# Kernel optimization log

Measured on AMD Instinct MI355X. Metric: run time of the kernel, lower is better.

## Reference

```python
import jax, jax.numpy as jnp
import numpy as np

B, T, H = 32, 512, 1024
I = 1024  # input_size == hidden_size


def _init_lstm(key, in_dim, hid):
    # PyTorch nn.LSTM init: U(-k, k), k = 1/sqrt(hidden_size)
    k = 1.0 / np.sqrt(hid)
    ks = jax.random.split(key, 4)
    Wih = jax.random.uniform(ks[0], (4 * hid, in_dim), minval=-k, maxval=k, dtype=jnp.float32)
    Whh = jax.random.uniform(ks[1], (4 * hid, hid), minval=-k, maxval=k, dtype=jnp.float32)
    bih = jax.random.uniform(ks[2], (4 * hid,), minval=-k, maxval=k, dtype=jnp.float32)
    bhh = jax.random.uniform(ks[3], (4 * hid,), minval=-k, maxval=k, dtype=jnp.float32)
    return Wih, Whh, bih, bhh


def setup_inputs() -> dict:
    key = jax.random.key(0)
    kx, k0, k1 = jax.random.split(key, 3)
    x = jax.random.normal(kx, (B, T, I), dtype=jnp.float32)
    Wih0, Whh0, bih0, bhh0 = _init_lstm(k0, I, H)
    Wih1, Whh1, bih1, bhh1 = _init_lstm(k1, H, H)
    return {"x": x, "Wih0": Wih0, "Whh0": Whh0, "bih0": bih0, "bhh0": bhh0,
            "Wih1": Wih1, "Whh1": Whh1, "bih1": bih1, "bhh1": bhh1}


def _lstm_layer(x, Wih, Whh, bih, bhh):
    # x: [B, T, in_dim] -> h_seq: [B, T, H]. PyTorch gate order: i, f, g, o.
    hid = Whh.shape[1]
    # Precompute input projections for all timesteps (one big GEMM).
    xg = jnp.einsum('bti,gi->btg', x, Wih) + bih + bhh  # [B, T, 4H]
    xg = jnp.swapaxes(xg, 0, 1)  # [T, B, 4H] for scan over time

    def step(carry, xg_t):
        h, c = carry
        gates = xg_t + h @ Whh.T  # [B, 4H]
        i, f, g, o = jnp.split(gates, 4, axis=-1)
        i = jax.nn.sigmoid(i)
        f = jax.nn.sigmoid(f)
        g = jnp.tanh(g)
        o = jax.nn.sigmoid(o)
        c = f * c + i * g
        h = o * jnp.tanh(c)
        return (h, c), h

    h0 = jnp.zeros((x.shape[0], hid), dtype=x.dtype)
    c0 = jnp.zeros((x.shape[0], hid), dtype=x.dtype)
    _, h_seq = jax.lax.scan(step, (h0, c0), xg)
    return jnp.swapaxes(h_seq, 0, 1)  # [B, T, H]


def reference(x, Wih0, Whh0, bih0, bhh0, Wih1, Whh1, bih1, bhh1):
    # Layer 0
    h = _lstm_layer(x, Wih0, Whh0, bih0, bhh0)
    # Layer 1 with residual add (dropout p=0.0 -> identity)
    h = h + _lstm_layer(h, Wih1, Whh1, bih1, bhh1)
    return h
```

## Files before the change

### kernel.cpp

```cpp
#include <hip/hip_runtime.h>
#include <hip/hip_bf16.h>

#define BB 32
#define TT 512
#define HH 1024
#define II 1024
#define G4H 4096
#define BH  (BB * HH)
#define HD  8
#define HMASK (HD - 1)

typedef __bf16 bf16x8_t __attribute__((ext_vector_type(8)));
typedef float f32x4_t __attribute__((ext_vector_type(4)));
typedef int i32x4_t __attribute__((ext_vector_type(4)));
typedef unsigned long long u64;

__device__ __forceinline__ void gload16(const void* g, void* l) {
    __builtin_amdgcn_global_load_lds(
        (const __attribute__((address_space(1))) unsigned int*)g,
        (__attribute__((address_space(3))) unsigned int*)l, 16, 0, 0);
}

__global__ void init_bufs(unsigned* __restrict__ h0w, unsigned* __restrict__ h1w,
                          unsigned* __restrict__ cnt) {
    int i = blockIdx.x * 256 + threadIdx.x;
    if (i < 16384)
        __hip_atomic_store(h0w + i, 0u, __ATOMIC_RELAXED, __HIP_MEMORY_SCOPE_AGENT);
    else if (i < 32768)
        __hip_atomic_store(h1w + (i - 16384), 0u, __ATOMIC_RELAXED, __HIP_MEMORY_SCOPE_AGENT);
    else if (i < 49152)
        __hip_atomic_store(cnt + (i - 32768), 0u, __ATOMIC_RELAXED, __HIP_MEMORY_SCOPE_AGENT);
}

__global__ void shuffle_w(const float* __restrict__ src, __hip_bfloat16* __restrict__ dst) {
    size_t i = (size_t)blockIdx.x * 256 + threadIdx.x;
    int jj   = (int)(i & 7);
    int lane = (int)((i >> 3) & 63);
    int kb   = (int)((i >> 9) & 15);
    int kh   = (int)((i >> 13) & 1);
    int tau  = (int)((i >> 14) & 1);
    int hg   = (int)(i >> 15);
    int n = lane & 15, q = lane >> 4;
    int row = (2 * tau + (n >> 3)) * 1024 + hg * 8 + (n & 7);
    int col = kh * 512 + kb * 32 + q * 8 + jj;
    dst[i] = __float2bfloat16(src[(size_t)row * II + col]);
}

__global__ void convert_x(const float* __restrict__ x, __hip_bfloat16* __restrict__ xb) {
    size_t i = (size_t)blockIdx.x * 256 + threadIdx.x;
    int ii = (int)(i & 1023);
    int b  = (int)((i >> 10) & 31);
    int t  = (int)(i >> 15);
    xb[i] = __float2bfloat16(x[((size_t)b * TT + t) * II + ii]);
}

__global__ __launch_bounds__(512, 2)
void lstm_persist(const __hip_bfloat16* __restrict__ xb,
                  const __hip_bfloat16* __restrict__ Wxs0, const __hip_bfloat16* __restrict__ Whs0,
                  const __hip_bfloat16* __restrict__ Wxs1, const __hip_bfloat16* __restrict__ Whs1,
                  const float* __restrict__ bih0, const float* __restrict__ bhh0,
                  const float* __restrict__ bih1, const float* __restrict__ bhh1,
                  __hip_bfloat16* __restrict__ h0seq,
                  __hip_bfloat16* __restrict__ h1seq,
                  float* __restrict__ out,
                  unsigned* __restrict__ cnt)
{
    const int wg = blockIdx.x, tid = threadIdx.x;
    const int bh = wg >> 7, hg = wg & 127;
    const int wave = tid >> 6, lane = tid & 63;
    const int L = wave >> 2, p = (wave >> 1) & 1, kh = wave & 1;
    const int n = lane & 15, q = lane >> 4;

    __shared__ float psum[2][2][2][16][37];
    __shared__ float res[2][128];
    __shared__ __align__(16) unsigned short hstage[2][16][8];
    __shared__ float houtf[16][8];
    __shared__ __align__(16) char astage[6 * 16384];

    const __hip_bfloat16* Wsel = L ? (p ? Whs1 : Wxs1) : (p ? Whs0 : Wxs0);
    const __bf16* wbp = (const __bf16*)Wsel;

    i32x4_t W0, W1, W2, W3, W4, W5, W6, W7, W8, W9, W10, W11, W12, W13, W14, W15,
            W16, W17, W18, W19, W20, W21, W22, W23, W24, W25, W26, W27, W28, W29, W30, W31;
#define LOADW(IDX, TAU, KB) \
    W##IDX = *(const i32x4_t*)(const void*)(wbp + ((((((size_t)hg * 2 + (TAU)) * 2 + kh) * 16) + (KB)) * 64 + lane) * 8)
    LOADW(0,0,0);  LOADW(1,0,1);  LOADW(2,0,2);  LOADW(3,0,3);
    LOADW(4,0,4);  LOADW(5,0,5);  LOADW(6,0,6);  LOADW(7,0,7);
    LOADW(8,0,8);  LOADW(9,0,9);  LOADW(10,0,10); LOADW(11,0,11);
    LOADW(12,0,12); LOADW(13,0,13); LOADW(14,0,14); LOADW(15,0,15);
    LOADW(16,1,0);  LOADW(17,1,1);  LOADW(18,1,2);  LOADW(19,1,3);
    LOADW(20,1,4);  LOADW(21,1,5);  LOADW(22,1,6);  LOADW(23,1,7);
    LOADW(24,1,8);  LOADW(25,1,9);  LOADW(26,1,10); LOADW(27,1,11);
    LOADW(28,1,12); LOADW(29,1,13); LOADW(30,1,14); LOADW(31,1,15);
#undef LOADW
    asm volatile("" : "+v"(W0), "+v"(W1), "+v"(W2), "+v"(W3),
                      "+v"(W4), "+v"(W5), "+v"(W6), "+v"(W7));
    asm volatile("" : "+v"(W8), "+v"(W9), "+v"(W10), "+v"(W11),
                      "+v"(W12), "+v"(W13), "+v"(W14), "+v"(W15));
    asm volatile("" : "+v"(W16), "+v"(W17), "+v"(W18), "+v"(W19),
                      "+v"(W20), "+v"(W21), "+v"(W22), "+v"(W23));
    asm volatile("" : "+v"(W24), "+v"(W25), "+v"(W26), "+v"(W27),
                      "+v"(W28), "+v"(W29), "+v"(W30), "+v"(W31));

    const int pw_L = tid >> 7, pw_idx = tid & 127, pw_b = (tid >> 3) & 15, pw_d = tid & 7;
    float bias_r[4] = {0.f, 0.f, 0.f, 0.f};
    float c_reg = 0.f;
    if (tid < 256) {
        const float* bi  = pw_L ? bih1 : bih0;
        const float* bh2 = pw_L ? bhh1 : bhh0;
#pragma unroll
        for (int g = 0; g < 4; ++g) {
            int row = g * 1024 + hg * 8 + pw_d;
            bias_r[g] = bi[row] + bh2[row];
        }
    }

    const int arow = bh * 16 + n;
    const bool is_master = (hg == bh);

    const int sread = (L == 0) ? (p == 0 ? kh : 2 + kh)
                               : (p == 0 ? 2 + kh : 4 + kh);
    const char* const rdbase = astage + sread * 16384 + lane * 16;

    if (wave == 0)
        asm volatile("buffer_inv sc0 sc1\n\ts_waitcnt vmcnt(0)" ::: "memory");
    __syncthreads();

    if (wave < 2) {
        const __bf16* gx = (const __bf16*)xb + arow * 1024 + kh * 512 + q * 8;
        char* ldx = astage + kh * 16384;
#pragma unroll
        for (int kb2 = 0; kb2 < 16; ++kb2)
            gload16(gx + kb2 * 32, ldx + kb2 * 1024);
    }

#define MSTEP(AV, IA, IB) \
    acc0 = __builtin_amdgcn_mfma_f32_16x16x32_bf16(AV, __builtin_bit_cast(bf16x8_t, W##IA), acc0, 0, 0, 0); \
    acc1 = __builtin_amdgcn_mfma_f32_16x16x32_bf16(AV, __builtin_bit_cast(bf16x8_t, W##IB), acc1, 0, 0, 0)
#define CSTEP(KB, IA, IB) { \
    bf16x8_t av = *(const bf16x8_t*)(const void*)(rdbase + (KB) * 1024); \
    MSTEP(av, IA, IB); }

    for (int t = 0; t <= TT; ++t) {
        if (p == 1) {
            const __hip_bfloat16* Ad = (L == 0)
                ? h0seq + (size_t)(t & HMASK) * BH
                : h1seq + (size_t)((t + HD - 1) & HMASK) * BH;
            const __bf16* gsrc = (const __bf16*)Ad + arow * 1024 + kh * 512 + q * 8;
            char* ldst = astage + ((L == 0 ? 2 : 4) + kh) * 16384;
#pragma unroll
            for (int kb2 = 0; kb2 < 16; ++kb2)
                gload16(gsrc + kb2 * 32, ldst + kb2 * 1024);
        }
        __syncthreads();

        f32x4_t acc0 = {0.f, 0.f, 0.f, 0.f};
        f32x4_t acc1 = {0.f, 0.f, 0.f, 0.f};
        CSTEP(0,0,16);  CSTEP(1,1,17);  CSTEP(2,2,18);  CSTEP(3,3,19);
        CSTEP(4,4,20);  CSTEP(5,5,21);  CSTEP(6,6,22);  CSTEP(7,7,23);
        CSTEP(8,8,24);  CSTEP(9,9,25);  CSTEP(10,10,26); CSTEP(11,11,27);
        CSTEP(12,12,28); CSTEP(13,13,29); CSTEP(14,14,30); CSTEP(15,15,31);

#pragma unroll
        for (int r = 0; r < 4; ++r) {
            psum[L][p][kh][q * 4 + r][n] = acc0[r];
            psum[L][p][kh][q * 4 + r][16 + n] = acc1[r];
        }
        __syncthreads();

        if (tid < 256) {
            const bool active = pw_L ? (t >= 1) : (t < TT);
            if (active) {
                float gv[4];
#pragma unroll
                for (int g = 0; g < 4; ++g) {
                    int col = (g >> 1) * 16 + (g & 1) * 8 + pw_d;
                    gv[g] = psum[pw_L][0][0][pw_b][col] + psum[pw_L][0][1][pw_b][col]
                          + psum[pw_L][1][0][pw_b][col] + psum[pw_L][1][1][pw_b][col]
                          + bias_r[g];
                }
                float si = 1.f / (1.f + __expf(-gv[0]));
                float sf = 1.f / (1.f + __expf(-gv[1]));
                float tg = 2.f / (1.f + __expf(-2.f * gv[2])) - 1.f;
                float so = 1.f / (1.f + __expf(-gv[3]));
                c_reg = sf * c_reg + si * tg;
                float hv = so * (2.f / (1.f + __expf(-2.f * c_reg)) - 1.f);
                __hip_bfloat16 hb16 = __float2bfloat16(hv);
                unsigned short hraw;
                __builtin_memcpy(&hraw, &hb16, 2);
                hstage[pw_L][pw_b][pw_d] = hraw;
                if (pw_L == 0) res[t & 1][pw_idx] = hv;
                else           houtf[pw_b][pw_d] = hv;
            }
        }
        __syncthreads();

        if (wave == 0) {
            if (tid < 32) {
                const int gl = tid >> 4, b = tid & 15;
                const bool go = gl ? (t >= 1) : (t < TT);
                if (go) {
                    i32x4_t hv16 = *(const i32x4_t*)(const void*)&hstage[gl][b][0];
                    const __hip_bfloat16* dst = gl
                        ? h1seq + ((size_t)(t & HMASK) * BH
                                   + (size_t)(bh * 16 + b) * 1024 + hg * 8)
                        : h0seq + ((size_t)((t + 1) & HMASK) * BH
                                   + (size_t)(bh * 16 + b) * 1024 + hg * 8);
                    asm volatile("global_store_dwordx4 %0, %1, off sc0 sc1"
                                 :: "v"((u64)dst), "v"(hv16) : "memory");
                }
            }
            asm volatile("s_waitcnt vmcnt(0)" ::: "memory");
            if (tid == 0 && t < TT)
                __hip_atomic_store(cnt + (size_t)wg * 32, (unsigned)(t + 1),
                                   __ATOMIC_RELAXED, __HIP_MEMORY_SCOPE_AGENT);
            if (t < TT) {
                const int tn = (t + 1 < TT) ? (t + 1) : (TT - 1);
                const __bf16* gx = (const __bf16*)xb + (size_t)tn * BH
                                   + arow * 1024 + q * 8;
                char* ldx = astage;
#pragma unroll
                for (int kb2 = 0; kb2 < 16; ++kb2)
                    gload16(gx + kb2 * 32, ldx + kb2 * 1024);
            }
        } else if (wave == 1) {
            if (t >= 1) {
                const int j = tid - 64;
                if (j < 32) {
                    const int b = j >> 1, hf = j & 1;
                    f32x4_t ov;
#pragma unroll
                    for (int k = 0; k < 4; ++k)
                        ov[k] = res[(t + 1) & 1][b * 8 + hf * 4 + k] + houtf[b][hf * 4 + k];
                    const float* dst = out + (size_t)(bh * 16 + b) * TT * HH
                                           + (size_t)(t - 1) * HH + hg * 8 + hf * 4;
                    asm volatile("global_store_dwordx4 %0, %1, off sc0 sc1"
                                 :: "v"((u64)dst), "v"(ov) : "memory");
                }
            }
            if (t < TT) {
                const int tn = (t + 1 < TT) ? (t + 1) : (TT - 1);
                const __bf16* gx = (const __bf16*)xb + (size_t)tn * BH
                                   + arow * 1024 + 512 + q * 8;
                char* ldx = astage + 16384;
#pragma unroll
                for (int kb2 = 0; kb2 < 16; ++kb2)
                    gload16(gx + kb2 * 32, ldx + kb2 * 1024);
            }
        }

        if (t < TT) {
            const unsigned tgt = (unsigned)(t + 1);
            if (is_master) {
                if (tid < 128) {
                    const unsigned* fl = cnt + (size_t)(bh * 128 + tid) * 32;
                    int spins = 0;
                    while (__hip_atomic_load(fl, __ATOMIC_RELAXED,
                                             __HIP_MEMORY_SCOPE_AGENT) < tgt
                           && spins < 8192) {
                        __builtin_amdgcn_s_sleep(1);
                        ++spins;
                    }
                }
                __syncthreads();
                if (tid < 16)
                    __hip_atomic_store(cnt + (size_t)(256 + bh * 16 + tid) * 32, tgt,
                                       __ATOMIC_RELAXED, __HIP_MEMORY_SCOPE_AGENT);
            } else {
                if (tid == 0) {
                    const unsigned* rl = cnt + (size_t)(256 + bh * 16 + (hg & 15)) * 32;
                    int spins = 0;
                    while (__hip_atomic_load(rl, __ATOMIC_RELAXED,
                                             __HIP_MEMORY_SCOPE_AGENT) < tgt
                           && spins < 8192) {
                        __builtin_amdgcn_s_sleep(1);
                        ++spins;
                    }
                }
                __syncthreads();
            }

            if (((t + 1) & HMASK) == 0) {
                if (wave == 0)
                    asm volatile("buffer_inv sc0 sc1\n\ts_waitcnt vmcnt(0)" ::: "memory");
                __syncthreads();
            }
        }
    }
#undef MSTEP
#undef CSTEP
}

extern "C" void kernel_launch(void* const* d_in, const int* in_sizes, int n_in,
                              void* d_out, int out_size, void* d_ws, size_t ws_size,
                              hipStream_t stream) {
    const float* x    = (const float*)d_in[0];
    const float* Wih0 = (const float*)d_in[1];
    const float* Whh0 = (const float*)d_in[2];
    const float* bih0 = (const float*)d_in[3];
    const float* bhh0 = (const float*)d_in[4];
    const float* Wih1 = (const float*)d_in[5];
    const float* Whh1 = (const float*)d_in[6];
    const float* bih1 = (const float*)d_in[7];
    const float* bhh1 = (const float*)d_in[8];
    float* out = (float*)d_out;
    (void)in_sizes; (void)n_in; (void)out_size; (void)ws_size;

    uint8_t* w = (uint8_t*)d_ws;
    const size_t WMAT = (size_t)G4H * HH * 2;
    __hip_bfloat16* Wxs0 = (__hip_bfloat16*)(w);
    __hip_bfloat16* Whs0 = (__hip_bfloat16*)(w + WMAT);
    __hip_bfloat16* Wxs1 = (__hip_bfloat16*)(w + 2 * WMAT);
    __hip_bfloat16* Whs1 = (__hip_bfloat16*)(w + 3 * WMAT);
    size_t off = 4 * WMAT;
    __hip_bfloat16* xbuf = (__hip_bfloat16*)(w + off); off += (size_t)TT * BB * II * 2;
    __hip_bfloat16* h0seq = (__hip_bfloat16*)(w + off); off += (size_t)HD * BH * 2;
    __hip_bfloat16* h1seq = (__hip_bfloat16*)(w + off); off += (size_t)HD * BH * 2;
    unsigned* cnt = (unsigned*)(w + off); off += 65536;

    init_bufs<<<256, 256, 0, stream>>>((unsigned*)h0seq, (unsigned*)h1seq, cnt);
    shuffle_w<<<(G4H * HH) / 256, 256, 0, stream>>>(Wih0, Wxs0);
    shuffle_w<<<(G4H * HH) / 256, 256, 0, stream>>>(Whh0, Whs0);
    shuffle_w<<<(G4H * HH) / 256, 256, 0, stream>>>(Wih1, Wxs1);
    shuffle_w<<<(G4H * HH) / 256, 256, 0, stream>>>(Whh1, Whs1);
    convert_x<<<(TT * BB * II) / 256, 256, 0, stream>>>(x, xbuf);

    lstm_persist<<<256, 512, 0, stream>>>(xbuf, Wxs0, Whs0, Wxs1, Whs1,
                                          bih0, bhh0, bih1, bhh1,
                                          h0seq, h1seq, out, cnt);
}
```

Baseline: 2.880 ms.

## Replace master-relay grid barrier with per-workgroup polling and skewed layer pipeline

Removes the two-hop master/relay inter-workgroup barrier. Four waves in every workgroup now poll the 128 peer counters directly and publish readiness through LDS flags. Layer 1 is skewed two phases behind layer 0, and its input projection reads the older h0 slot from a separate LDS buffer, so each wave waits only for the data it needs instead of a full barrier. This aims to cut barrier latency per timestep. It adds polling traffic and more LDS, and the wider ring-buffer indexing adds risk of correctness errors.

Measured after the change: 3.132 ms. 8.7% more time.

```diff
diff --git a/kernel.cpp b/kernel.cpp
--- a/kernel.cpp
+++ b/kernel.cpp
@@ -9,6 +9,7 @@
 #define BH  (BB * HH)
 #define HD  8
 #define HMASK (HD - 1)
+#define NPH (TT + 2)
 
 typedef __bf16 bf16x8_t __attribute__((ext_vector_type(8)));
 typedef float f32x4_t __attribute__((ext_vector_type(4)));
@@ -27,9 +28,13 @@
     if (i < 16384)
         __hip_atomic_store(h0w + i, 0u, __ATOMIC_RELAXED, __HIP_MEMORY_SCOPE_AGENT);
     else if (i < 32768)
-        __hip_atomic_store(h1w + (i - 16384), 0u, __ATOMIC_RELAXED, __HIP_MEMORY_SCOPE_AGENT);
+        __hip_atomic_store(h1w + 7 * 16384 + (i - 16384), 0u,
+                           __ATOMIC_RELAXED, __HIP_MEMORY_SCOPE_AGENT);
     else if (i < 49152)
         __hip_atomic_store(cnt + (i - 32768), 0u, __ATOMIC_RELAXED, __HIP_MEMORY_SCOPE_AGENT);
+    else
+        __hip_atomic_store(cnt + 16384 + (i - 49152), 0u,
+                           __ATOMIC_RELAXED, __HIP_MEMORY_SCOPE_AGENT);
 }
 
 __global__ void shuffle_w(const float* __restrict__ src, __hip_bfloat16* __restrict__ dst) {
@@ -72,10 +77,14 @@
     const int n = lane & 15, q = lane >> 4;
 
     __shared__ float psum[2][2][2][16][37];
-    __shared__ float res[2][128];
+    __shared__ float res[4][128];
     __shared__ __align__(16) unsigned short hstage[2][16][8];
     __shared__ float houtf[16][8];
-    __shared__ __align__(16) char astage[6 * 16384];
+    __shared__ __align__(16) char ax[2][16384];
+    __shared__ __align__(16) char ah0c[2][16384];
+    __shared__ __align__(16) char ah0o[2][16384];
+    __shared__ __align__(16) char ah1[2][16384];
+    __shared__ unsigned lds_rel[4];
 
     const __hip_bfloat16* Wsel = L ? (p ? Whs1 : Wxs1) : (p ? Whs0 : Wxs0);
     const __bf16* wbp = (const __bf16*)Wsel;
@@ -116,60 +125,116 @@
     }
 
     const int arow = bh * 16 + n;
-    const bool is_master = (hg == bh);
-
-    const int sread = (L == 0) ? (p == 0 ? kh : 2 + kh)
-                               : (p == 0 ? 2 + kh : 4 + kh);
-    const char* const rdbase = astage + sread * 16384 + lane * 16;
+    const bool pollw = (wave == 2 || wave == 3 || wave == 6 || wave == 7);
+    const int pidx = (wave == 2) ? 0 : (wave == 3) ? 1 : (wave == 6) ? 2 : 3;
 
     if (wave == 0)
         asm volatile("buffer_inv sc0 sc1\n\ts_waitcnt vmcnt(0)" ::: "memory");
-    __syncthreads();
-
+    if (tid < 4) lds_rel[tid] = 0u;
     if (wave < 2) {
         const __bf16* gx = (const __bf16*)xb + arow * 1024 + kh * 512 + q * 8;
-        char* ldx = astage + kh * 16384;
+        char* ldx = ax[kh];
 #pragma unroll
         for (int kb2 = 0; kb2 < 16; ++kb2)
             gload16(gx + kb2 * 32, ldx + kb2 * 1024);
     }
-
-#define MSTEP(AV, IA, IB) \
-    acc0 = __builtin_amdgcn_mfma_f32_16x16x32_bf16(AV, __builtin_bit_cast(bf16x8_t, W##IA), acc0, 0, 0, 0); \
-    acc1 = __builtin_amdgcn_mfma_f32_16x16x32_bf16(AV, __builtin_bit_cast(bf16x8_t, W##IB), acc1, 0, 0, 0)
+    __syncthreads();
+
+#define MFMA16(AV, WB, ACC) \
+    __builtin_amdgcn_mfma_f32_16x16x32_bf16(AV, __builtin_bit_cast(bf16x8_t, WB), ACC, 0, 0, 0)
 #define CSTEP(KB, IA, IB) { \
-    bf16x8_t av = *(const bf16x8_t*)(const void*)(rdbase + (KB) * 1024); \
-    MSTEP(av, IA, IB); }
-
-    for (int t = 0; t <= TT; ++t) {
-        if (p == 1) {
-            const __hip_bfloat16* Ad = (L == 0)
-                ? h0seq + (size_t)(t & HMASK) * BH
-                : h1seq + (size_t)((t + HD - 1) & HMASK) * BH;
-            const __bf16* gsrc = (const __bf16*)Ad + arow * 1024 + kh * 512 + q * 8;
-            char* ldst = astage + ((L == 0 ? 2 : 4) + kh) * 16384;
+    bf16x8_t av = *(const bf16x8_t*)(const void*)(rb + (KB) * 1024); \
+    acc0 = MFMA16(av, W##IA, acc0); acc1 = MFMA16(av, W##IB, acc1); }
+
+    for (int u = 0; u < NPH; ++u) {
+        const bool g0run = (L == 0) && (u < TT);
+        const bool g1run = (L == 1) && (u >= 2);
+
+        if (pollw) {
+            const unsigned tgt = (unsigned)u;
+            if (lane < 32) {
+                const unsigned* fl = cnt + (size_t)(bh * 128 + pidx * 32 + lane) * 32;
+                int sp = 0;
+                while (__hip_atomic_load(fl, __ATOMIC_RELAXED,
+                                         __HIP_MEMORY_SCOPE_AGENT) < tgt
+                       && sp < 8192) { __builtin_amdgcn_s_sleep(1); ++sp; }
+            }
+            if (lane == 0)
+                __hip_atomic_store(&lds_rel[pidx], tgt,
+                                   __ATOMIC_RELAXED, __HIP_MEMORY_SCOPE_WORKGROUP);
+            int sp = 0;
+            for (;;) {
+                unsigned m0 = __hip_atomic_load(&lds_rel[0], __ATOMIC_RELAXED, __HIP_MEMORY_SCOPE_WORKGROUP);
+                unsigned m1 = __hip_atomic_load(&lds_rel[1], __ATOMIC_RELAXED, __HIP_MEMORY_SCOPE_WORKGROUP);
+                unsigned m2 = __hip_atomic_load(&lds_rel[2], __ATOMIC_RELAXED, __HIP_MEMORY_SCOPE_WORKGROUP);
+                unsigned m3 = __hip_atomic_load(&lds_rel[3], __ATOMIC_RELAXED, __HIP_MEMORY_SCOPE_WORKGROUP);
+                if ((m0 >= tgt && m1 >= tgt && m2 >= tgt && m3 >= tgt) || sp >= 16384) break;
+                __builtin_amdgcn_s_sleep(1); ++sp;
+            }
+        } else if ((wave == 4 || wave == 5) && g1run) {
+            const unsigned tgt = (unsigned)(u - 1);
+            int sp = 0;
+            for (;;) {
+                unsigned m0 = __hip_atomic_load(&lds_rel[0], __ATOMIC_RELAXED, __HIP_MEMORY_SCOPE_WORKGROUP);
+                unsigned m1 = __hip_atomic_load(&lds_rel[1], __ATOMIC_RELAXED, __HIP_MEMORY_SCOPE_WORKGROUP);
+                unsigned m2 = __hip_atomic_load(&lds_rel[2], __ATOMIC_RELAXED, __HIP_MEMORY_SCOPE_WORKGROUP);
+                unsigned m3 = __hip_atomic_load(&lds_rel[3], __ATOMIC_RELAXED, __HIP_MEMORY_SCOPE_WORKGROUP);
+                if ((m0 >= tgt && m1 >= tgt && m2 >= tgt && m3 >= tgt) || sp >= 16384) break;
+                __builtin_amdgcn_s_sleep(1); ++sp;
+            }
+        }
+
+        if (g0run && p == 1) {
+            const __bf16* gsrc = (const __bf16*)h0seq + (size_t)(u & HMASK) * BH
+                                 + arow * 1024 + kh * 512 + q * 8;
+            char* ldst = ah0c[kh];
 #pragma unroll
             for (int kb2 = 0; kb2 < 16; ++kb2)
                 gload16(gsrc + kb2 * 32, ldst + kb2 * 1024);
+            asm volatile("s_waitcnt vmcnt(0)" ::: "memory");
+            __builtin_amdgcn_sched_barrier(0);
+        } else if (g1run && p == 0) {
+            const __bf16* gsrc = (const __bf16*)h0seq + (size_t)((u + 7) & HMASK) * BH
+                                 + arow * 1024 + kh * 512 + q * 8;
+            char* ldst = ah0o[kh];
+#pragma unroll
+            for (int kb2 = 0; kb2 < 16; ++kb2)
+                gload16(gsrc + kb2 * 32, ldst + kb2 * 1024);
+            asm volatile("s_waitcnt vmcnt(0)" ::: "memory");
+            __builtin_amdgcn_sched_barrier(0);
+        } else if (g1run && p == 1) {
+            const __bf16* gsrc = (const __bf16*)h1seq + (size_t)((u + 5) & HMASK) * BH
+                                 + arow * 1024 + kh * 512 + q * 8;
+            char* ldst = ah1[kh];
+#pragma unroll
+            for (int kb2 = 0; kb2 < 16; ++kb2)
+                gload16(gsrc + kb2 * 32, ldst + kb2 * 1024);
+            asm volatile("s_waitcnt vmcnt(0)" ::: "memory");
+            __builtin_amdgcn_sched_barrier(0);
+        } else if (g0run && p == 0) {
+            asm volatile("s_waitcnt vmcnt(0)" ::: "memory");
+            __builtin_amdgcn_sched_barrier(0);
+        }
+
+        if (g0run || g1run) {
+            const char* rb = (L == 0 ? (p == 0 ? ax[kh] : ah0c[kh])
+                                     : (p == 0 ? ah0o[kh] : ah1[kh])) + lane * 16;
+            f32x4_t acc0 = {0.f, 0.f, 0.f, 0.f};
+            f32x4_t acc1 = {0.f, 0.f, 0.f, 0.f};
+            CSTEP(0,0,16);  CSTEP(1,1,17);  CSTEP(2,2,18);  CSTEP(3,3,19);
+            CSTEP(4,4,20);  CSTEP(5,5,21);  CSTEP(6,6,22);  CSTEP(7,7,23);
+            CSTEP(8,8,24);  CSTEP(9,9,25);  CSTEP(10,10,26); CSTEP(11,11,27);
+            CSTEP(12,12,28); CSTEP(13,13,29); CSTEP(14,14,30); CSTEP(15,15,31);
+#pragma unroll
+            for (int r = 0; r < 4; ++r) {
+                psum[L][p][kh][q * 4 + r][n] = acc0[r];
+                psum[L][p][kh][q * 4 + r][16 + n] = acc1[r];
+            }
         }
         __syncthreads();
 
-        f32x4_t acc0 = {0.f, 0.f, 0.f, 0.f};
-        f32x4_t acc1 = {0.f, 0.f, 0.f, 0.f};
-        CSTEP(0,0,16);  CSTEP(1,1,17);  CSTEP(2,2,18);  CSTEP(3,3,19);
-        CSTEP(4,4,20);  CSTEP(5,5,21);  CSTEP(6,6,22);  CSTEP(7,7,23);
-        CSTEP(8,8,24);  CSTEP(9,9,25);  CSTEP(10,10,26); CSTEP(11,11,27);
-        CSTEP(12,12,28); CSTEP(13,13,29); CSTEP(14,14,30); CSTEP(15,15,31);
-
-#pragma unroll
-        for (int r = 0; r < 4; ++r) {
-            psum[L][p][kh][q * 4 + r][n] = acc0[r];
-            psum[L][p][kh][q * 4 + r][16 + n] = acc1[r];
-        }
-        __syncthreads();
-
         if (tid < 256) {
-            const bool active = pw_L ? (t >= 1) : (t < TT);
+            const bool active = pw_L ? (u >= 2) : (u < TT);
             if (active) {
                 float gv[4];
 #pragma unroll
@@ -189,7 +254,7 @@
                 unsigned short hraw;
                 __builtin_memcpy(&hraw, &hb16, 2);
                 hstage[pw_L][pw_b][pw_d] = hraw;
-                if (pw_L == 0) res[t & 1][pw_idx] = hv;
+                if (pw_L == 0) res[u & 3][pw_idx] = hv;
                 else           houtf[pw_b][pw_d] = hv;
             }
         }
@@ -198,96 +263,61 @@
         if (wave == 0) {
             if (tid < 32) {
                 const int gl = tid >> 4, b = tid & 15;
-                const bool go = gl ? (t >= 1) : (t < TT);
+                const bool go = gl ? (u >= 2) : (u < TT);
                 if (go) {
                     i32x4_t hv16 = *(const i32x4_t*)(const void*)&hstage[gl][b][0];
                     const __hip_bfloat16* dst = gl
-                        ? h1seq + ((size_t)(t & HMASK) * BH
+                        ? h1seq + ((size_t)((u - 2) & HMASK) * BH
                                    + (size_t)(bh * 16 + b) * 1024 + hg * 8)
-                        : h0seq + ((size_t)((t + 1) & HMASK) * BH
+                        : h0seq + ((size_t)((u + 1) & HMASK) * BH
                                    + (size_t)(bh * 16 + b) * 1024 + hg * 8);
                     asm volatile("global_store_dwordx4 %0, %1, off sc0 sc1"
                                  :: "v"((u64)dst), "v"(hv16) : "memory");
                 }
             }
             asm volatile("s_waitcnt vmcnt(0)" ::: "memory");
-            if (tid == 0 && t < TT)
-                __hip_atomic_store(cnt + (size_t)wg * 32, (unsigned)(t + 1),
+            if (tid == 0 && u <= TT)
+                __hip_atomic_store(cnt + (size_t)wg * 32, (unsigned)(u + 1),
                                    __ATOMIC_RELAXED, __HIP_MEMORY_SCOPE_AGENT);
-            if (t < TT) {
-                const int tn = (t + 1 < TT) ? (t + 1) : (TT - 1);
-                const __bf16* gx = (const __bf16*)xb + (size_t)tn * BH
+            if (u + 1 < TT) {
+                const __bf16* gx = (const __bf16*)xb + (size_t)(u + 1) * BH
                                    + arow * 1024 + q * 8;
-                char* ldx = astage;
 #pragma unroll
                 for (int kb2 = 0; kb2 < 16; ++kb2)
-                    gload16(gx + kb2 * 32, ldx + kb2 * 1024);
+                    gload16(gx + kb2 * 32, ax[0] + kb2 * 1024);
             }
         } else if (wave == 1) {
-            if (t >= 1) {
+            if (u >= 2) {
                 const int j = tid - 64;
                 if (j < 32) {
                     const int b = j >> 1, hf = j & 1;
                     f32x4_t ov;
 #pragma unroll
                     for (int k = 0; k < 4; ++k)
-                        ov[k] = res[(t + 1) & 1][b * 8 + hf * 4 + k] + houtf[b][hf * 4 + k];
+                        ov[k] = res[(u - 2) & 3][b * 8 + hf * 4 + k] + houtf[b][hf * 4 + k];
                     const float* dst = out + (size_t)(bh * 16 + b) * TT * HH
-                                           + (size_t)(t - 1) * HH + hg * 8 + hf * 4;
+                                           + (size_t)(u - 2) * HH + hg * 8 + hf * 4;
                     asm volatile("global_store_dwordx4 %0, %1, off sc0 sc1"
                                  :: "v"((u64)dst), "v"(ov) : "memory");
                 }
             }
-            if (t < TT) {
-                const int tn = (t + 1 < TT) ? (t + 1) : (TT - 1);
-                const __bf16* gx = (const __bf16*)xb + (size_t)tn * BH
+            if (u + 1 < TT) {
+                const __bf16* gx = (const __bf16*)xb + (size_t)(u + 1) * BH
                                    + arow * 1024 + 512 + q * 8;
-                char* ldx = astage + 16384;
 #pragma unroll
                 for (int kb2 = 0; kb2 < 16; ++kb2)
-                    gload16(gx + kb2 * 32, ldx + kb2 * 1024);
-            }
-        }
-
-        if (t < TT) {
-            const unsigned tgt = (unsigned)(t + 1);
-            if (is_master) {
-                if (tid < 128) {
-                    const unsigned* fl = cnt + (size_t)(bh * 128 + tid) * 32;
-                    int spins = 0;
-                    while (__hip_atomic_load(fl, __ATOMIC_RELAXED,
-                                             __HIP_MEMORY_SCOPE_AGENT) < tgt
-                           && spins < 8192) {
-                        __builtin_amdgcn_s_sleep(1);
-                        ++spins;
-                    }
-                }
-                __syncthreads();
-                if (tid < 16)
-                    __hip_atomic_store(cnt + (size_t)(256 + bh * 16 + tid) * 32, tgt,
-                                       __ATOMIC_RELAXED, __HIP_MEMORY_SCOPE_AGENT);
-            } else {
-                if (tid == 0) {
-                    const unsigned* rl = cnt + (size_t)(256 + bh * 16 + (hg & 15)) * 32;
-                    int spins = 0;
-                    while (__hip_atomic_load(rl, __ATOMIC_RELAXED,
-                                             __HIP_MEMORY_SCOPE_AGENT) < tgt
-                           && spins < 8192) {
-                        __builtin_amdgcn_s_sleep(1);
-                        ++spins;
-                    }
-                }
-                __syncthreads();
-            }
-
-            if (((t + 1) & HMASK) == 0) {
-                if (wave == 0)
-                    asm volatile("buffer_inv sc0 sc1\n\ts_waitcnt vmcnt(0)" ::: "memory");
-                __syncthreads();
-            }
+                    gload16(gx + kb2 * 32, ax[1] + kb2 * 1024);
+            }
+        }
+
+        if (((u + 1) & HMASK) == 0 && (u + 1) < NPH) {
+            __syncthreads();
+            if (wave == 0)
+                asm volatile("buffer_inv sc0 sc1\n\ts_waitcnt vmcnt(0)" ::: "memory");
+            __syncthreads();
         }
     }
-#undef MSTEP
+#undef MFMA16
 #undef CSTEP
 }
 
@@ -316,7 +346,7 @@
     __hip_bfloat16* xbuf = (__hip_bfloat16*)(w + off); off += (size_t)TT * BB * II * 2;
     __hip_bfloat16* h0seq = (__hip_bfloat16*)(w + off); off += (size_t)HD * BH * 2;
     __hip_bfloat16* h1seq = (__hip_bfloat16*)(w + off); off += (size_t)HD * BH * 2;
-    unsigned* cnt = (unsigned*)(w + off); off += 65536;
+    unsigned* cnt = (unsigned*)(w + off); off += 131072;
 
     init_bufs<<<256, 256, 0, stream>>>((unsigned*)h0seq, (unsigned*)h1seq, cnt);
     shuffle_w<<<(G4H * HH) / 256, 256, 0, stream>>>(Wih0, Wxs0);
```
